# Kernel optimization log

Hardware: AMD Instinct MI355X
Metric: run time of the kernel (lower is better)

The kernel has to match this reference:

```python
import jax, jax.numpy as jnp
import numpy as np

C = 256
G = 16
EPS = 1e-5


def conv1x1(x, w):
    # x: [N,C,H,W], w: [Cout,Cin]
    return jnp.einsum('nchw,oc->nohw', x, w)


def group_norm(x, gamma, beta, groups=G, eps=EPS):
    n, c, h, w = x.shape
    xg = x.reshape(n, groups, c // groups, h, w)
    mu = xg.mean(axis=(2, 3, 4), keepdims=True)
    var = ((xg - mu) ** 2).mean(axis=(2, 3, 4), keepdims=True)
    xn = ((xg - mu) * jax.lax.rsqrt(var + eps)).reshape(n, c, h, w)
    return xn * gamma[:, None, None] + beta[:, None, None]


def silu(x):
    return x * jax.nn.sigmoid(x)


def scan(x, axis, reverse=False):
    if reverse:
        return jnp.flip(jnp.cumsum(jnp.flip(x, axis), axis=axis), axis)
    return jnp.cumsum(x, axis=axis)


def depthwise3x3(x, w_dw):
    # w_dw: [C,1,3,3], groups=C
    return jax.lax.conv_general_dilated(
        x, w_dw, window_strides=(1, 1), padding=((1, 1), (1, 1)),
        dimension_numbers=('NCHW', 'OIHW', 'NCHW'), feature_group_count=x.shape[1])


def setup_inputs() -> dict:
    key = jax.random.key(0)
    ks = jax.random.split(key, 5)
    N, H, W = 8, 80, 80
    s1 = 1.0 / np.sqrt(C)
    return {
        'x': jax.random.normal(ks[0], (N, C, H, W), jnp.float32),
        'w_pre': jax.random.normal(ks[1], (C, C), jnp.float32) * s1,
        'g1': jnp.ones((C,), jnp.float32),
        'b1': jnp.zeros((C,), jnp.float32),
        'w_gate': jax.random.normal(ks[2], (C, C), jnp.float32) * s1,
        'b_gate': jnp.zeros((C,), jnp.float32),
        'w_dw': jax.random.normal(ks[3], (C, 1, 3, 3), jnp.float32) * (1.0 / 3.0),
        'w_pw': jax.random.normal(ks[4], (C, C), jnp.float32) * s1,
        'g2': jnp.ones((C,), jnp.float32),
        'b2': jnp.zeros((C,), jnp.float32),
    }


def reference(x, w_pre, g1, b1, w_gate, b_gate, w_dw, w_pw, g2, b2):
    # pre: 1x1 conv -> GroupNorm -> SiLU
    h = silu(group_norm(conv1x1(x, w_pre), g1, b1))
    # 4-directional cumulative scans
    lr = scan(h, 3, False)
    rl = scan(h, 3, True)
    tb = scan(h, 2, False)
    bt = scan(h, 2, True)
    fused = (lr + rl + tb + bt) * 0.25
    # sigmoid gate from pre features
    gate = jax.nn.sigmoid(conv1x1(h, w_gate) + b_gate[:, None, None])
    gated = fused * gate
    # mix: depthwise 3x3 -> 1x1 -> GroupNorm -> SiLU
    y = depthwise3x3(gated, w_dw)
    y = conv1x1(y, w_pw)
    return silu(group_norm(y, g2, b2))
```

## Files before the change

### kernel.cpp

```cpp
#include <hip/hip_runtime.h>
#include <stdint.h>

#define CC 256
#define HH 80
#define WW 80
#define PP 6400
#define GG 16
#define GNCNT (16*6400)
#define SAPAD 272

using frag_ab = __attribute__((ext_vector_type(8))) short;
using frag_cd = __attribute__((ext_vector_type(4))) float;
typedef unsigned short u16;

__device__ __forceinline__ float b2f(u16 u) {
    union { float f; uint32_t i; } v; v.i = ((uint32_t)u) << 16; return v.f;
}
__device__ __forceinline__ u16 f2b(float f) {
    uint32_t x = __float_as_uint(f);
    return (u16)((x + 0x7fffu + ((x >> 16) & 1u)) >> 16);
}
__device__ __forceinline__ float sigf(float x) { return 1.f / (1.f + __expf(-x)); }

__global__ __launch_bounds__(256) void cvt_kernel(const float* __restrict__ src,
                                                  u16* __restrict__ dst, int n4) {
    int i = blockIdx.x * 256 + threadIdx.x;
    if (i < n4) {
        float4 v = ((const float4*)src)[i];
        ushort4 o;
        o.x = f2b(v.x); o.y = f2b(v.y); o.z = f2b(v.z); o.w = f2b(v.w);
        ((ushort4*)dst)[i] = o;
    }
}

__global__ __launch_bounds__(256) void cvtT_kernel(const float* __restrict__ x,
                                                   u16* __restrict__ Xt) {
    __shared__ u16 sT[64 * 72];
    const int p0 = blockIdx.x * 64, c0 = blockIdx.y * 64, n = blockIdx.z;
    const int t = threadIdx.x;
    {
        const int cl = t >> 2, pq = t & 3;
        const float* row = x + ((size_t)(n * CC + c0 + cl)) * PP + p0 + pq * 16;
        #pragma unroll
        for (int u = 0; u < 4; u++) {
            float4 v = ((const float4*)(row + u * 4))[0];
            const int pp = pq * 16 + u * 4;
            sT[(pp + 0) * 72 + cl] = f2b(v.x);
            sT[(pp + 1) * 72 + cl] = f2b(v.y);
            sT[(pp + 2) * 72 + cl] = f2b(v.z);
            sT[(pp + 3) * 72 + cl] = f2b(v.w);
        }
    }
    __syncthreads();
    {
        const int pl = t >> 2, cq = t & 3;
        u16* orow = Xt + ((size_t)(n * PP + p0 + pl)) * CC + c0 + cq * 16;
        *(frag_ab*)(orow)     = *(const frag_ab*)(sT + pl * 72 + cq * 16);
        *(frag_ab*)(orow + 8) = *(const frag_ab*)(sT + pl * 72 + cq * 16 + 8);
    }
}

template<int MODE>
__global__ __launch_bounds__(256, 2) void gemm_kernel(
    const u16* __restrict__ A,
    const u16* __restrict__ Wb,
    u16* __restrict__ Out,
    float* __restrict__ pstats,
    const u16* __restrict__ Hb,
    const float* __restrict__ Srow,
    const float* __restrict__ Scol,
    const float* __restrict__ bgate)
{
    __shared__ __align__(16) u16 sA[64 * SAPAD];

    const int t    = threadIdx.x;
    const int lane = t & 63;
    const int wave = t >> 6;
    const int m    = lane & 15;
    const int q    = lane >> 4;
    const int mt   = blockIdx.x;
    const int m0   = mt * 64;
    const int n    = mt / 100;
    const int o0w  = wave * 64;

    {
        const int row = t >> 2, qt = t & 3;
        const u16* g = A + (size_t)(m0 + row) * CC + qt * 64;
        u16* d = sA + row * SAPAD + qt * 64;
        #pragma unroll
        for (int i = 0; i < 8; i++)
            *(frag_ab*)(d + i * 8) = *(const frag_ab*)(g + i * 8);
    }
    __syncthreads();

    frag_cd acc[4][4];
    #pragma unroll
    for (int ms = 0; ms < 4; ms++)
        #pragma unroll
        for (int j = 0; j < 4; j++)
            #pragma unroll
            for (int k = 0; k < 4; k++) acc[ms][j][k] = 0.f;

    const u16* wl = Wb + (size_t)(o0w + m) * CC + q * 8;

    #pragma unroll
    for (int jh = 0; jh < 2; jh++) {
        frag_ab wf[2][8];
        #pragma unroll
        for (int jj = 0; jj < 2; jj++)
            #pragma unroll
            for (int kc = 0; kc < 8; kc++)
                wf[jj][kc] = *(const frag_ab*)(wl + (size_t)((jh * 2 + jj) * 16) * CC + kc * 32);
        #pragma unroll
        for (int jj = 0; jj < 2; jj++)
            #pragma unroll
            for (int kc = 0; kc < 8; kc++)
                asm volatile("" : "+v"(wf[jj][kc]));

        #pragma unroll
        for (int ms = 0; ms < 4; ms++) {
            #pragma unroll
            for (int kc = 0; kc < 8; kc++) {
                frag_ab af = *(const frag_ab*)(sA + (ms * 16 + m) * SAPAD + kc * 32 + q * 8);
                #pragma unroll
                for (int jj = 0; jj < 2; jj++)
                    acc[ms][jh * 2 + jj] = __builtin_amdgcn_mfma_f32_16x16x32_bf16(
                        af, wf[jj][kc], acc[ms][jh * 2 + jj], 0, 0, 0);
            }
        }
    }
    __syncthreads();

    if (MODE == 0 || MODE == 2) {
        #pragma unroll
        for (int j = 0; j < 4; j++) {
            float s = 0.f, sq = 0.f;
            #pragma unroll
            for (int ms = 0; ms < 4; ms++)
                #pragma unroll
                for (int r = 0; r < 4; r++) {
                    float v = acc[ms][j][r];
                    s += v; sq += v * v;
                }
            #pragma unroll
            for (int off = 32; off > 0; off >>= 1) {
                s  += __shfl_down(s, off);
                sq += __shfl_down(sq, off);
            }
            if (lane == 0) {
                float* p = pstats + (size_t)mt * 32;
                p[wave * 4 + j]      = s;
                p[16 + wave * 4 + j] = sq;
            }
        }
        u16* myT = sA + wave * 1152;
        #pragma unroll
        for (int ms = 0; ms < 4; ms++) {
            #pragma unroll
            for (int j = 0; j < 4; j++)
                #pragma unroll
                for (int r = 0; r < 4; r++)
                    myT[(q * 4 + r) * 72 + j * 16 + m] = f2b(acc[ms][j][r]);
            #pragma unroll
            for (int u = 0; u < 2; u++) {
                const int rr = u * 8 + (lane >> 3);
                frag_ab v = *(const frag_ab*)(myT + rr * 72 + (lane & 7) * 8);
                *(frag_ab*)(Out + (size_t)(m0 + ms * 16 + rr) * CC + o0w + (lane & 7) * 8) = v;
            }
        }
    } else {
        float* myG = (float*)sA + wave * 1152;
        float bg[4];
        #pragma unroll
        for (int j = 0; j < 4; j++) bg[j] = bgate[o0w + j * 16 + m];
        #pragma unroll
        for (int ms = 0; ms < 4; ms++) {
            #pragma unroll
            for (int j = 0; j < 4; j++)
                #pragma unroll
                for (int r = 0; r < 4; r++)
                    myG[(q * 4 + r) * 72 + j * 16 + m] = sigf(acc[ms][j][r] + bg[j]);
            #pragma unroll
            for (int u = 0; u < 4; u++) {
                const int rr  = u * 4 + (lane >> 4);
                const int col = (lane & 15) * 4;
                float4 g4 = *(const float4*)(myG + rr * 72 + col);
                const int row = m0 + ms * 16 + rr;
                const int pl  = row - n * PP;
                const int pr  = pl / WW;
                const int pc  = pl - pr * WW;
                const int o   = o0w + col;
                ushort4 hv = *(const ushort4*)(Hb + (size_t)row * CC + o);
                float4  sr = *(const float4*)(Srow + (size_t)(n * HH + pr) * CC + o);
                float4  sc = *(const float4*)(Scol + (size_t)(n * HH + pc) * CC + o);
                ushort4 ov;
                ov.x = f2b(0.25f * (sr.x + sc.x + 2.f * b2f(hv.x)) * g4.x);
                ov.y = f2b(0.25f * (sr.y + sc.y + 2.f * b2f(hv.y)) * g4.y);
                ov.z = f2b(0.25f * (sr.z + sc.z + 2.f * b2f(hv.z)) * g4.z);
                ov.w = f2b(0.25f * (sr.w + sc.w + 2.f * b2f(hv.w)) * g4.w);
                *(ushort4*)(Out + (size_t)row * CC + o) = ov;
            }
        }
    }
}

__global__ __launch_bounds__(256) void reduce_stats_kernel(
    const float* __restrict__ pscr, float* __restrict__ stats_out)
{
    const int t = threadIdx.x;
    const int g = t & 15, n = (t >> 4) & 7, kind = t >> 7;
    float s = 0.f;
    #pragma unroll 4
    for (int i = 0; i < 100; i++)
        s += pscr[(size_t)(n * 100 + i) * 32 + kind * 16 + g];
    stats_out[t] = s;
}

__global__ __launch_bounds__(256) void gn1_kernel(
    const u16* __restrict__ c1, u16* __restrict__ hb,
    float* __restrict__ Srow,
    const float* __restrict__ stats,
    const float* __restrict__ g1, const float* __restrict__ b1)
{
    __shared__ float sred[8 * 256];
    const int i = blockIdx.x, n = blockIdx.y;
    const int t = threadIdx.x;
    const int jg = t >> 5, cc = t & 31;
    const int c8 = cc * 8;
    const int g  = cc >> 1;
    const float su   = stats[n * GG + g];
    const float sq   = stats[128 + n * GG + g];
    const float mean = su * (1.f / GNCNT);
    const float var  = sq * (1.f / GNCNT) - mean * mean;
    const float inv  = rsqrtf(var + 1e-5f);
    float a[8], b[8];
    #pragma unroll
    for (int k = 0; k < 8; k++) {
        a[k] = inv * g1[c8 + k];
        b[k] = b1[c8 + k] - mean * a[k];
    }
    float srow8[8];
    #pragma unroll
    for (int k = 0; k < 8; k++) srow8[k] = 0.f;

    const size_t base = (size_t)(n * PP + i * WW) * CC;
    for (int s = 0; s < 10; s++) {
        const int j = jg + s * 8;
        const u16* src = c1 + base + (size_t)j * CC + c8;
        u16*       dst = hb + base + (size_t)j * CC + c8;
        frag_ab v = *(const frag_ab*)src;
        frag_ab o;
        #pragma unroll
        for (int k = 0; k < 8; k++) {
            float xn = b2f((u16)v[k]) * a[k] + b[k];
            float hs = xn * sigf(xn);
            o[k] = (short)f2b(hs);
            srow8[k] += hs;
        }
        *(frag_ab*)dst = o;
    }
    #pragma unroll
    for (int k = 0; k < 8; k++) sred[jg * 256 + c8 + k] = srow8[k];
    __syncthreads();
    {
        const int c = t;
        float s = 0.f;
        #pragma unroll
        for (int k = 0; k < 8; k++) s += sred[k * 256 + c];
        Srow[(size_t)(n * HH + i) * CC + c] = s;
    }
}

__global__ __launch_bounds__(256) void scol_kernel(
    const u16* __restrict__ hb, float* __restrict__ Scol)
{
    const int jg = blockIdx.x, iq = blockIdx.y, n = blockIdx.z;
    const int t = threadIdx.x;
    const int js = t >> 5, cc = t & 31;
    const int j = jg * 8 + js, c8 = cc * 8;
    float acc8[8];
    #pragma unroll
    for (int k = 0; k < 8; k++) acc8[k] = 0.f;
    for (int s = 0; s < 20; s++) {
        const int i = iq * 20 + s;
        frag_ab v = *(const frag_ab*)(hb + (size_t)(n * PP + i * WW + j) * CC + c8);
        #pragma unroll
        for (int k = 0; k < 8; k++) acc8[k] += b2f((u16)v[k]);
    }
    float* dst = Scol + (size_t)(n * HH + j) * CC + c8;
    #pragma unroll
    for (int k = 0; k < 8; k++) atomicAdd(&dst[k], acc8[k]);
}

__global__ __launch_bounds__(256) void dw_kernel(
    const u16* __restrict__ gin, u16* __restrict__ dout,
    const float* __restrict__ wdw)
{
    __shared__ float sw[1152];
    const int i = blockIdx.x, chalf = blockIdx.y, n = blockIdx.z;
    const int t = threadIdx.x;
    for (int u = t; u < 1152; u += 256) sw[u] = wdw[chalf * 1152 + u];
    __syncthreads();

    const int jg = t >> 5, cc = t & 31;
    const int gc = chalf * 128 + cc * 4;
    float wl[4][9];
    #pragma unroll
    for (int cl = 0; cl < 4; cl++)
        #pragma unroll
        for (int k = 0; k < 9; k++) wl[cl][k] = sw[(cc * 4 + cl) * 9 + k];

    const size_t nbase = (size_t)n * PP * CC;
    for (int s = 0; s < 10; s++) {
        const int j = jg + s * 8;
        float acc4[4] = {0.f, 0.f, 0.f, 0.f};
        #pragma unroll
        for (int di = -1; di <= 1; di++) {
            const int ii = i + di;
            if (ii < 0 || ii >= HH) continue;
            #pragma unroll
            for (int dj = -1; dj <= 1; dj++) {
                const int jj = j + dj;
                if (jj < 0 || jj >= WW) continue;
                ushort4 v = *(const ushort4*)(gin + nbase + (size_t)(ii * WW + jj) * CC + gc);
                const int k = (di + 1) * 3 + (dj + 1);
                acc4[0] += wl[0][k] * b2f(v.x);
                acc4[1] += wl[1][k] * b2f(v.y);
                acc4[2] += wl[2][k] * b2f(v.z);
                acc4[3] += wl[3][k] * b2f(v.w);
            }
        }
        ushort4 o;
        o.x = f2b(acc4[0]); o.y = f2b(acc4[1]); o.z = f2b(acc4[2]); o.w = f2b(acc4[3]);
        *(ushort4*)(dout + nbase + (size_t)(i * WW + j) * CC + gc) = o;
    }
}

__global__ __launch_bounds__(256) void gn2T_kernel(
    const u16* __restrict__ Y, float* __restrict__ out,
    const float* __restrict__ stats,
    const float* __restrict__ g2, const float* __restrict__ b2v)
{
    __shared__ u16 sT[64 * 72];
    const int p0 = blockIdx.x * 64, c0 = blockIdx.y * 64, n = blockIdx.z;
    const int t = threadIdx.x;
    {
        const int pl = t >> 2, cq = t & 3;
        const u16* row = Y + (size_t)(n * PP + p0 + pl) * CC + c0 + cq * 16;
        *(frag_ab*)(sT + pl * 72 + cq * 16)     = *(const frag_ab*)(row);
        *(frag_ab*)(sT + pl * 72 + cq * 16 + 8) = *(const frag_ab*)(row + 8);
    }
    __syncthreads();
    {
        const int cl = t >> 2, pq = t & 3;
        const int c = c0 + cl, g = c >> 4;
        const float su   = stats[256 + n * GG + g];
        const float sq   = stats[384 + n * GG + g];
        const float mean = su * (1.f / GNCNT);
        const float var  = sq * (1.f / GNCNT) - mean * mean;
        const float inv  = rsqrtf(var + 1e-5f);
        const float a    = inv * g2[c];
        const float b    = b2v[c] - mean * a;
        float* orow = out + (size_t)(n * CC + c) * PP + p0 + pq * 16;
        #pragma unroll
        for (int u4 = 0; u4 < 4; u4++) {
            float4 o;
            float* op = (float*)&o;
            #pragma unroll
            for (int e = 0; e < 4; e++) {
                const int pp = pq * 16 + u4 * 4 + e;
                float xn = b2f(sT[pp * 72 + cl]) * a + b;
                op[e] = xn * sigf(xn);
            }
            ((float4*)(orow + u4 * 4))[0] = o;
        }
    }
}

extern "C" void kernel_launch(void* const* d_in, const int* in_sizes, int n_in,
                              void* d_out, int out_size, void* d_ws, size_t ws_size,
                              hipStream_t stream)
{
    const float* x      = (const float*)d_in[0];
    const float* w_pre  = (const float*)d_in[1];
    const float* g1     = (const float*)d_in[2];
    const float* b1     = (const float*)d_in[3];
    const float* w_gate = (const float*)d_in[4];
    const float* b_gate = (const float*)d_in[5];
    const float* w_dw   = (const float*)d_in[6];
    const float* w_pw   = (const float*)d_in[7];
    const float* g2     = (const float*)d_in[8];
    const float* b2     = (const float*)d_in[9];
    float* out = (float*)d_out;

    char* ws = (char*)d_ws;
    u16*   wb0   = (u16*)(ws);
    u16*   wb1   = (u16*)(ws + 131072);
    u16*   wb2   = (u16*)(ws + 262144);
    u16*   Xt    = (u16*)(ws + 393216);
    u16*   bufA  = (u16*)(ws + 26607616);
    u16*   bufB  = (u16*)(ws + 52822016);
    float* Srow  = (float*)(ws + 79036416);
    float* Scol  = (float*)(ws + 79691776);
    float* stats = (float*)(ws + 80347136);

    float* pscr0 = (float*)bufB;
    float* pscr1 = (float*)Xt;

    hipMemsetAsync(Scol, 0, 655360, stream);

    cvt_kernel<<<64, 256, 0, stream>>>(w_pre,  wb0, 16384);
    cvt_kernel<<<64, 256, 0, stream>>>(w_gate, wb1, 16384);
    cvt_kernel<<<64, 256, 0, stream>>>(w_pw,   wb2, 16384);
    cvtT_kernel<<<dim3(100, 4, 8), 256, 0, stream>>>(x, Xt);

    gemm_kernel<0><<<800, 256, 0, stream>>>(Xt, wb0, bufA, pscr0,
                                            nullptr, nullptr, nullptr, nullptr);
    reduce_stats_kernel<<<1, 256, 0, stream>>>(pscr0, stats);
    gn1_kernel<<<dim3(80, 8), 256, 0, stream>>>(bufA, bufB, Srow, stats, g1, b1);
    scol_kernel<<<dim3(10, 4, 8), 256, 0, stream>>>(bufB, Scol);
    gemm_kernel<1><<<800, 256, 0, stream>>>(bufB, wb1, bufA, nullptr,
                                            bufB, Srow, Scol, b_gate);
    dw_kernel<<<dim3(80, 2, 8), 256, 0, stream>>>(bufA, bufB, w_dw);
    gemm_kernel<2><<<800, 256, 0, stream>>>(bufB, wb2, bufA, pscr1,
                                            nullptr, nullptr, nullptr, nullptr);
    reduce_stats_kernel<<<1, 256, 0, stream>>>(pscr1, stats + 256);
    gn2T_kernel<<<dim3(100, 4, 8), 256, 0, stream>>>(bufA, out, stats, g2, b2);
}
```

Measured before the change: 319.5 us.

## Fuse input transpose into first GEMM and stats reduction into GN kernels

The first GEMM now reads fp32 NCHW input directly, converting and transposing it into shared memory. This removes the separate cvtT kernel and the Xt buffer round trip. The per-tile GroupNorm partial sums are reduced inside gn1/gn2T instead of in dedicated single-block reduce kernels, which drops two launches at the cost of redundant reductions per block. The gate GEMM reuses the H tile already staged in shared memory rather than reloading it from global, and launch bounds rise to 3 blocks per SM, which may pressure registers.

New measurement: 305.6 us. -4.4%, faster.

```diff
diff --git a/kernel.cpp b/kernel.cpp
--- a/kernel.cpp
+++ b/kernel.cpp
@@ -33,43 +33,16 @@
     }
 }
 
-__global__ __launch_bounds__(256) void cvtT_kernel(const float* __restrict__ x,
-                                                   u16* __restrict__ Xt) {
-    __shared__ u16 sT[64 * 72];
-    const int p0 = blockIdx.x * 64, c0 = blockIdx.y * 64, n = blockIdx.z;
-    const int t = threadIdx.x;
-    {
-        const int cl = t >> 2, pq = t & 3;
-        const float* row = x + ((size_t)(n * CC + c0 + cl)) * PP + p0 + pq * 16;
-        #pragma unroll
-        for (int u = 0; u < 4; u++) {
-            float4 v = ((const float4*)(row + u * 4))[0];
-            const int pp = pq * 16 + u * 4;
-            sT[(pp + 0) * 72 + cl] = f2b(v.x);
-            sT[(pp + 1) * 72 + cl] = f2b(v.y);
-            sT[(pp + 2) * 72 + cl] = f2b(v.z);
-            sT[(pp + 3) * 72 + cl] = f2b(v.w);
-        }
-    }
-    __syncthreads();
-    {
-        const int pl = t >> 2, cq = t & 3;
-        u16* orow = Xt + ((size_t)(n * PP + p0 + pl)) * CC + c0 + cq * 16;
-        *(frag_ab*)(orow)     = *(const frag_ab*)(sT + pl * 72 + cq * 16);
-        *(frag_ab*)(orow + 8) = *(const frag_ab*)(sT + pl * 72 + cq * 16 + 8);
-    }
-}
-
 template<int MODE>
-__global__ __launch_bounds__(256, 2) void gemm_kernel(
+__global__ __launch_bounds__(256, 3) void gemm_kernel(
     const u16* __restrict__ A,
     const u16* __restrict__ Wb,
     u16* __restrict__ Out,
     float* __restrict__ pstats,
-    const u16* __restrict__ Hb,
     const float* __restrict__ Srow,
     const float* __restrict__ Scol,
-    const float* __restrict__ bgate)
+    const float* __restrict__ bgate,
+    const float* __restrict__ Xf)
 {
     __shared__ __align__(16) u16 sA[64 * SAPAD];
 
@@ -83,7 +56,24 @@
     const int n    = mt / 100;
     const int o0w  = wave * 64;
 
-    {
+    if (MODE == 0) {
+        const int cl = t >> 2, pq = t & 3;
+        const int p0 = m0 - n * PP;
+        #pragma unroll
+        for (int cb = 0; cb < 4; cb++) {
+            const int c = cb * 64 + cl;
+            const float* row = Xf + ((size_t)(n * CC + c)) * PP + p0 + pq * 16;
+            #pragma unroll
+            for (int u = 0; u < 4; u++) {
+                float4 v = ((const float4*)(row + u * 4))[0];
+                const int pp = pq * 16 + u * 4;
+                sA[(pp + 0) * SAPAD + c] = f2b(v.x);
+                sA[(pp + 1) * SAPAD + c] = f2b(v.y);
+                sA[(pp + 2) * SAPAD + c] = f2b(v.z);
+                sA[(pp + 3) * SAPAD + c] = f2b(v.w);
+            }
+        }
+    } else {
         const int row = t >> 2, qt = t & 3;
         const u16* g = A + (size_t)(m0 + row) * CC + qt * 64;
         u16* d = sA + row * SAPAD + qt * 64;
@@ -128,6 +118,17 @@
                         af, wf[jj][kc], acc[ms][jh * 2 + jj], 0, 0, 0);
             }
         }
+    }
+
+    ushort4 hv[4][4];
+    if (MODE == 1) {
+        const int rr0 = lane >> 4;
+        const int cH  = o0w + (lane & 15) * 4;
+        #pragma unroll
+        for (int ms = 0; ms < 4; ms++)
+            #pragma unroll
+            for (int u = 0; u < 4; u++)
+                hv[ms][u] = *(const ushort4*)(sA + (size_t)(ms * 16 + u * 4 + rr0) * SAPAD + cH);
     }
     __syncthreads();
 
@@ -190,46 +191,45 @@
                 const int pr  = pl / WW;
                 const int pc  = pl - pr * WW;
                 const int o   = o0w + col;
-                ushort4 hv = *(const ushort4*)(Hb + (size_t)row * CC + o);
+                ushort4 hq = hv[ms][u];
                 float4  sr = *(const float4*)(Srow + (size_t)(n * HH + pr) * CC + o);
                 float4  sc = *(const float4*)(Scol + (size_t)(n * HH + pc) * CC + o);
                 ushort4 ov;
-                ov.x = f2b(0.25f * (sr.x + sc.x + 2.f * b2f(hv.x)) * g4.x);
-                ov.y = f2b(0.25f * (sr.y + sc.y + 2.f * b2f(hv.y)) * g4.y);
-                ov.z = f2b(0.25f * (sr.z + sc.z + 2.f * b2f(hv.z)) * g4.z);
-                ov.w = f2b(0.25f * (sr.w + sc.w + 2.f * b2f(hv.w)) * g4.w);
+                ov.x = f2b(0.25f * (sr.x + sc.x + 2.f * b2f(hq.x)) * g4.x);
+                ov.y = f2b(0.25f * (sr.y + sc.y + 2.f * b2f(hq.y)) * g4.y);
+                ov.z = f2b(0.25f * (sr.z + sc.z + 2.f * b2f(hq.z)) * g4.z);
+                ov.w = f2b(0.25f * (sr.w + sc.w + 2.f * b2f(hq.w)) * g4.w);
                 *(ushort4*)(Out + (size_t)row * CC + o) = ov;
             }
         }
     }
-}
-
-__global__ __launch_bounds__(256) void reduce_stats_kernel(
-    const float* __restrict__ pscr, float* __restrict__ stats_out)
-{
-    const int t = threadIdx.x;
-    const int g = t & 15, n = (t >> 4) & 7, kind = t >> 7;
-    float s = 0.f;
-    #pragma unroll 4
-    for (int i = 0; i < 100; i++)
-        s += pscr[(size_t)(n * 100 + i) * 32 + kind * 16 + g];
-    stats_out[t] = s;
 }
 
 __global__ __launch_bounds__(256) void gn1_kernel(
     const u16* __restrict__ c1, u16* __restrict__ hb,
     float* __restrict__ Srow,
-    const float* __restrict__ stats,
+    const float* __restrict__ pscr,
     const float* __restrict__ g1, const float* __restrict__ b1)
 {
     __shared__ float sred[8 * 256];
+    __shared__ float sstat[32];
     const int i = blockIdx.x, n = blockIdx.y;
     const int t = threadIdx.x;
+    if (t < 32) {
+        const int kind = t >> 4, g = t & 15;
+        const float* p = pscr + (size_t)(n * 100) * 32 + kind * 16 + g;
+        float s = 0.f;
+        #pragma unroll 4
+        for (int ii = 0; ii < 100; ii++) s += p[ii * 32];
+        sstat[t] = s;
+    }
+    __syncthreads();
+
     const int jg = t >> 5, cc = t & 31;
     const int c8 = cc * 8;
     const int g  = cc >> 1;
-    const float su   = stats[n * GG + g];
-    const float sq   = stats[128 + n * GG + g];
+    const float su   = sstat[g];
+    const float sq   = sstat[16 + g];
     const float mean = su * (1.f / GNCNT);
     const float var  = sq * (1.f / GNCNT) - mean * mean;
     const float inv  = rsqrtf(var + 1e-5f);
@@ -338,12 +338,21 @@
 
 __global__ __launch_bounds__(256) void gn2T_kernel(
     const u16* __restrict__ Y, float* __restrict__ out,
-    const float* __restrict__ stats,
+    const float* __restrict__ pscr,
     const float* __restrict__ g2, const float* __restrict__ b2v)
 {
     __shared__ u16 sT[64 * 72];
+    __shared__ float sstat[32];
     const int p0 = blockIdx.x * 64, c0 = blockIdx.y * 64, n = blockIdx.z;
     const int t = threadIdx.x;
+    if (t < 32) {
+        const int kind = t >> 4, g = t & 15;
+        const float* p = pscr + (size_t)(n * 100) * 32 + kind * 16 + g;
+        float s = 0.f;
+        #pragma unroll 4
+        for (int ii = 0; ii < 100; ii++) s += p[ii * 32];
+        sstat[t] = s;
+    }
     {
         const int pl = t >> 2, cq = t & 3;
         const u16* row = Y + (size_t)(n * PP + p0 + pl) * CC + c0 + cq * 16;
@@ -354,8 +363,8 @@
     {
         const int cl = t >> 2, pq = t & 3;
         const int c = c0 + cl, g = c >> 4;
-        const float su   = stats[256 + n * GG + g];
-        const float sq   = stats[384 + n * GG + g];
+        const float su   = sstat[g];
+        const float sq   = sstat[16 + g];
         const float mean = su * (1.f / GNCNT);
         const float var  = sq * (1.f / GNCNT) - mean * mean;
         const float inv  = rsqrtf(var + 1e-5f);
@@ -397,33 +406,27 @@
     u16*   wb0   = (u16*)(ws);
     u16*   wb1   = (u16*)(ws + 131072);
     u16*   wb2   = (u16*)(ws + 262144);
-    u16*   Xt    = (u16*)(ws + 393216);
     u16*   bufA  = (u16*)(ws + 26607616);
     u16*   bufB  = (u16*)(ws + 52822016);
     float* Srow  = (float*)(ws + 79036416);
     float* Scol  = (float*)(ws + 79691776);
-    float* stats = (float*)(ws + 80347136);
-
-    float* pscr0 = (float*)bufB;
-    float* pscr1 = (float*)Xt;
+    float* pscr0 = (float*)(ws + 80347136);
+    float* pscr1 = (float*)(ws + 80449536);
 
     hipMemsetAsync(Scol, 0, 655360, stream);
 
     cvt_kernel<<<64, 256, 0, stream>>>(w_pre,  wb0, 16384);
     cvt_kernel<<<64, 256, 0, stream>>>(w_gate, wb1, 16384);
     cvt_kernel<<<64, 256, 0, stream>>>(w_pw,   wb2, 16384);
-    cvtT_kernel<<<dim3(100, 4, 8), 256, 0, stream>>>(x, Xt);
-
-    gemm_kernel<0><<<800, 256, 0, stream>>>(Xt, wb0, bufA, pscr0,
-                                            nullptr, nullptr, nullptr, nullptr);
-    reduce_stats_kernel<<<1, 256, 0, stream>>>(pscr0, stats);
-    gn1_kernel<<<dim3(80, 8), 256, 0, stream>>>(bufA, bufB, Srow, stats, g1, b1);
+
+    gemm_kernel<0><<<800, 256, 0, stream>>>(nullptr, wb0, bufA, pscr0,
+                                            nullptr, nullptr, nullptr, x);
+    gn1_kernel<<<dim3(80, 8), 256, 0, stream>>>(bufA, bufB, Srow, pscr0, g1, b1);
     scol_kernel<<<dim3(10, 4, 8), 256, 0, stream>>>(bufB, Scol);
     gemm_kernel<1><<<800, 256, 0, stream>>>(bufB, wb1, bufA, nullptr,
-                                            bufB, Srow, Scol, b_gate);
+                                            Srow, Scol, b_gate, nullptr);
     dw_kernel<<<dim3(80, 2, 8), 256, 0, stream>>>(bufA, bufB, w_dw);
     gemm_kernel<2><<<800, 256, 0, stream>>>(bufB, wb2, bufA, pscr1,
                                             nullptr, nullptr, nullptr, nullptr);
-    reduce_stats_kernel<<<1, 256, 0, stream>>>(pscr1, stats + 256);
-    gn2T_kernel<<<dim3(100, 4, 8), 256, 0, stream>>>(bufA, out, stats, g2, b2);
-}
+    gn2T_kernel<<<dim3(100, 4, 8), 256, 0, stream>>>(bufA, out, pscr1, g2, b2);
+}
```
